# Kernel tuning notes

Measured on AMD Instinct MI355X. Metric: run time of the kernel, lower is better.

Reference implementation:

```python
import jax, jax.numpy as jnp
import numpy as np

B, K, D, NH = 4096, 32, 1024, 16
HD = D // NH
LN_EPS = 1e-5
RMS_EPS = 1e-6


def layernorm(x, g, b):
    mu = jnp.mean(x, axis=-1, keepdims=True)
    var = jnp.mean((x - mu) ** 2, axis=-1, keepdims=True)
    return (x - mu) * jax.lax.rsqrt(var + LN_EPS) * g + b


def rmsnorm(x, g):
    ms = jnp.mean(x ** 2, axis=-1, keepdims=True)
    return x * jax.lax.rsqrt(ms + RMS_EPS) * g


def setup_inputs() -> dict:
    key = jax.random.key(0)
    ks = jax.random.split(key, 12)
    s = 0.02
    inp = {
        "query": jax.random.normal(ks[0], (B, D), jnp.float32),
        "point_features": jax.random.normal(ks[1], (B, K, D), jnp.float32),
        "lnq_g": jnp.ones((D,), jnp.float32),
        "lnq_b": jnp.zeros((D,), jnp.float32),
        "lnkv_g": jnp.ones((D,), jnp.float32),
        "lnkv_b": jnp.zeros((D,), jnp.float32),
        "Wq": jax.random.normal(ks[2], (D, D), jnp.float32) * s,
        "bq": jnp.zeros((D,), jnp.float32),
        "Wk": jax.random.normal(ks[3], (D, D), jnp.float32) * s,
        "bk": jnp.zeros((D,), jnp.float32),
        "Wv": jax.random.normal(ks[4], (D, D), jnp.float32) * s,
        "bv": jnp.zeros((D,), jnp.float32),
        "rmsq_g": jnp.ones((D,), jnp.float32),
        "rmsk_g": jnp.ones((D,), jnp.float32),
        "Wo": jax.random.normal(ks[5], (D, D), jnp.float32) * s,
        "bo": jnp.zeros((D,), jnp.float32),
        "mlpn_g": jnp.ones((D,), jnp.float32),
        "mlpn_b": jnp.zeros((D,), jnp.float32),
        "W1": jax.random.normal(ks[6], (D, 4 * D), jnp.float32) * s,
        "b1": jnp.zeros((4 * D,), jnp.float32),
        "W2": jax.random.normal(ks[7], (4 * D, D), jnp.float32) * s,
        "b2": jnp.zeros((D,), jnp.float32),
    }
    return inp


def reference(query, point_features, lnq_g, lnq_b, lnkv_g, lnkv_b,
              Wq, bq, Wk, bk, Wv, bv, rmsq_g, rmsk_g, Wo, bo,
              mlpn_g, mlpn_b, W1, b1, W2, b2):
    q_in = layernorm(query, lnq_g, lnq_b)            # [B, D]
    kv_in = layernorm(point_features, lnkv_g, lnkv_b)  # [B, K, D]

    q = rmsnorm(q_in @ Wq + bq, rmsq_g)              # [B, D]
    k = rmsnorm(kv_in @ Wk + bk, rmsk_g)             # [B, K, D]
    v = kv_in @ Wv + bv                               # [B, K, D]

    # Faithful to original: raw row-major reshape [B,K,D] -> [B,NH,K,HD]
    qh = q.reshape(B, NH, HD)                         # [B, NH, HD] (q_len = 1)
    kh = k.reshape(B, NH, K, HD)
    vh = v.reshape(B, NH, K, HD)

    scores = jnp.einsum('bhd,bhkd->bhk', qh, kh) / np.sqrt(HD).astype(np.float32)
    attn = jax.nn.softmax(scores, axis=-1)            # [B, NH, K]
    out = jnp.einsum('bhk,bhkd->bhd', attn, vh)       # [B, NH, HD]

    # Faithful: transpose(1,2) then reshape -> [B, HD, NH] -> [B, D]
    out = jnp.transpose(out, (0, 2, 1)).reshape(B, D)
    out = (out @ Wo + bo) + query                     # residual

    h = layernorm(out, mlpn_g, mlpn_b)
    mlp_out = (jax.nn.gelu(h @ W1 + b1, approximate=False) @ W2) + b2
    return out + mlp_out
```

## Files before the change

kernel.cpp:

```cpp
#include <hip/hip_runtime.h>
#include <stdint.h>

#define DEVI __device__ __forceinline__

typedef unsigned short u16;
typedef short s8v __attribute__((ext_vector_type(8)));
typedef float f4v __attribute__((ext_vector_type(4)));
typedef u16 u16x4 __attribute__((ext_vector_type(4)));

DEVI u16 f2bf(float f) {
  unsigned u = __float_as_uint(f);
  u += 0x7fffu + ((u >> 16) & 1u);
  return (u16)(u >> 16);
}
DEVI float bf2f(u16 h) { return __uint_as_float(((unsigned)h) << 16); }

DEVI void gload16(const void* g, void* l) {
  __builtin_amdgcn_global_load_lds(
      (const __attribute__((address_space(1))) void*)(uintptr_t)g,
      (__attribute__((address_space(3))) void*)(uintptr_t)l, 16, 0, 0);
}

__global__ __launch_bounds__(256) void transpose_w(const float* __restrict__ W,
                                                   u16* __restrict__ Wt, int R, int C) {
  __shared__ float tile[32][33];
  const int tx = threadIdx.x & 31, ty = threadIdx.x >> 5;
  const int r0 = blockIdx.y * 32, c0 = blockIdx.x * 32;
#pragma unroll
  for (int i = 0; i < 4; ++i)
    tile[ty + 8 * i][tx] = W[(size_t)(r0 + ty + 8 * i) * C + c0 + tx];
  __syncthreads();
#pragma unroll
  for (int i = 0; i < 4; ++i)
    Wt[(size_t)(c0 + ty + 8 * i) * R + r0 + tx] = f2bf(tile[tx][ty + 8 * i]);
}

__global__ __launch_bounds__(256) void ln_rows(const float* __restrict__ x,
                                               const float* __restrict__ g,
                                               const float* __restrict__ bsh,
                                               u16* __restrict__ y,
                                               float* __restrict__ zbuf) {
  const size_t row = blockIdx.x;
  const int t = threadIdx.x;
  if (zbuf && t == 0) zbuf[row] = 0.f;
  float4 v = ((const float4*)(x + row * 1024))[t];
  float s = v.x + v.y + v.z + v.w;
  float q = v.x * v.x + v.y * v.y + v.z * v.z + v.w * v.w;
#pragma unroll
  for (int m = 1; m < 64; m <<= 1) { s += __shfl_xor(s, m); q += __shfl_xor(q, m); }
  __shared__ float sh[8];
  if ((t & 63) == 0) { sh[t >> 6] = s; sh[4 + (t >> 6)] = q; }
  __syncthreads();
  s = sh[0] + sh[1] + sh[2] + sh[3];
  q = sh[4] + sh[5] + sh[6] + sh[7];
  const float mu = s * (1.f / 1024.f);
  const float var = q * (1.f / 1024.f) - mu * mu;
  const float rs = rsqrtf(var + 1e-5f);
  const int c = t * 4;
  const float in[4] = {v.x, v.y, v.z, v.w};
  u16x4 o;
#pragma unroll
  for (int i = 0; i < 4; ++i) o[i] = f2bf((in[i] - mu) * rs * g[c + i] + bsh[c + i]);
  *(u16x4*)(y + row * 1024 + c) = o;
}

template <int EPI>
__global__ __launch_bounds__(512, 2) void gemm256(
    const u16* __restrict__ A, const u16* __restrict__ Bt,
    const float* __restrict__ biasK, const float* __restrict__ biasV,
    const float* __restrict__ gcol, u16* __restrict__ CK, u16* __restrict__ CV,
    float* __restrict__ rowssq, int M, int N, int K, int RB, int CB) {
  __shared__ u16 lds[4][16384];
  const int t = threadIdx.x;
  const int lane = t & 63;
  const int wave = t >> 6;
  const int wm = wave >> 2, wn = wave & 3;
  const int fr = lane & 15, kq = lane >> 4;

  const int bid = blockIdx.x;
  const int cpx = gridDim.x >> 3;
  const int swz = (bid & 7) * cpx + (bid >> 3);
  const int rb = swz / CB, cb = swz % CB;
  const size_t row0 = (size_t)rb * 256, col0 = (size_t)cb * 256;

  f4v acc[8][4];
#pragma unroll
  for (int i = 0; i < 8; ++i)
#pragma unroll
    for (int n = 0; n < 4; ++n) acc[i][n] = (f4v){0.f, 0.f, 0.f, 0.f};

  const u16* Ag0 = A + (row0 + (t >> 2)) * (size_t)K + (t & 3) * 8;
  const u16* Ag1 = Ag0 + (size_t)128 * K;
  const u16* Bg0 = Bt + (col0 + (t >> 2)) * (size_t)K + (t & 3) * 8;
  const u16* Bg1 = Bg0 + (size_t)128 * K;

  const int NT = K >> 5;

#pragma unroll
  for (int tt = 0; tt < 3; ++tt) {
    u16* sA = &lds[tt][0];
    u16* sB = &lds[tt][8192];
    gload16(Ag0 + tt * 32, sA + t * 8);
    gload16(Ag1 + tt * 32, sA + 4096 + t * 8);
    gload16(Bg0 + tt * 32, sB + t * 8);
    gload16(Bg1 + tt * 32, sB + 4096 + t * 8);
  }

#pragma unroll 4
  for (int T = 0; T < NT; ++T) {
    asm volatile("s_waitcnt vmcnt(8)" ::: "memory");
    __builtin_amdgcn_s_barrier();
    __builtin_amdgcn_sched_barrier(0);
    const u16* sA = &lds[T & 3][0];
    const u16* sB = &lds[T & 3][8192];
    const int Ts = (T + 3 < NT) ? T + 3 : NT - 1;
    s8v a[4], b[4];
#pragma unroll
    for (int m = 0; m < 4; ++m)
      a[m] = *(const s8v*)&sA[(wm * 128 + m * 16 + fr) * 32 + kq * 8];
#pragma unroll
    for (int n = 0; n < 4; ++n)
      b[n] = *(const s8v*)&sB[(wn * 64 + n * 16 + fr) * 32 + kq * 8];
    {
      u16* dA = &lds[(T + 3) & 3][0];
      gload16(Ag0 + Ts * 32, dA + t * 8);
      gload16(Ag1 + Ts * 32, dA + 4096 + t * 8);
    }
    __builtin_amdgcn_s_setprio(1);
#pragma unroll
    for (int m = 0; m < 4; ++m)
#pragma unroll
      for (int n = 0; n < 4; ++n)
        acc[m][n] = __builtin_amdgcn_mfma_f32_16x16x32_bf16(a[m], b[n], acc[m][n], 0, 0, 0);
    __builtin_amdgcn_s_setprio(0);
    __builtin_amdgcn_s_barrier();
#pragma unroll
    for (int m = 0; m < 4; ++m)
      a[m] = *(const s8v*)&sA[(wm * 128 + 64 + m * 16 + fr) * 32 + kq * 8];
    {
      u16* dB = &lds[(T + 3) & 3][8192];
      gload16(Bg0 + Ts * 32, dB + t * 8);
      gload16(Bg1 + Ts * 32, dB + 4096 + t * 8);
    }
    __builtin_amdgcn_s_setprio(1);
#pragma unroll
    for (int m = 0; m < 4; ++m)
#pragma unroll
      for (int n = 0; n < 4; ++n)
        acc[4 + m][n] = __builtin_amdgcn_mfma_f32_16x16x32_bf16(a[m], b[n], acc[4 + m][n], 0, 0, 0);
    __builtin_amdgcn_s_setprio(0);
  }

  const int kq4 = kq * 4;
  if (EPI == 0) {
    const bool isK = (col0 < 1024);
    if (isK) {
#pragma unroll
      for (int ai = 0; ai < 8; ++ai) {
        int cols[4];
        float bb[4], gg[4];
#pragma unroll
        for (int n = 0; n < 4; ++n) {
          cols[n] = (int)col0 + wn * 64 + n * 16 + fr;
          bb[n] = biasK[cols[n]];
          gg[n] = gcol[cols[n]];
        }
#pragma unroll
        for (int r = 0; r < 4; ++r) {
          const size_t grow = row0 + wm * 128 + ai * 16 + kq4 + r;
          float v[4];
#pragma unroll
          for (int n = 0; n < 4; ++n) v[n] = acc[ai][n][r] + bb[n];
          float s = v[0] * v[0] + v[1] * v[1] + v[2] * v[2] + v[3] * v[3];
          s += __shfl_xor(s, 1);
          s += __shfl_xor(s, 2);
          s += __shfl_xor(s, 4);
          s += __shfl_xor(s, 8);
          if (fr == 0) atomicAdd(&rowssq[grow], s);
#pragma unroll
          for (int n = 0; n < 4; ++n)
            CK[grow * 1024 + cols[n]] = f2bf(v[n] * gg[n]);
        }
      }
    } else {
#pragma unroll
      for (int ai = 0; ai < 8; ++ai) {
        int cols[4];
        float bb[4];
#pragma unroll
        for (int n = 0; n < 4; ++n) {
          cols[n] = (int)col0 - 1024 + wn * 64 + n * 16 + fr;
          bb[n] = biasV[cols[n]];
        }
#pragma unroll
        for (int r = 0; r < 4; ++r) {
          const size_t grow = row0 + wm * 128 + ai * 16 + kq4 + r;
#pragma unroll
          for (int n = 0; n < 4; ++n)
            CV[grow * 1024 + cols[n]] = f2bf(acc[ai][n][r] + bb[n]);
        }
      }
    }
  } else {
#pragma unroll
    for (int ai = 0; ai < 8; ++ai) {
      int cols[4];
      float bb[4];
#pragma unroll
      for (int n = 0; n < 4; ++n) {
        cols[n] = (int)col0 + wn * 64 + n * 16 + fr;
        bb[n] = biasK[cols[n]];
      }
#pragma unroll
      for (int r = 0; r < 4; ++r) {
        const size_t grow = row0 + wm * 128 + ai * 16 + kq4 + r;
#pragma unroll
        for (int n = 0; n < 4; ++n) {
          const float x = acc[ai][n][r] + bb[n];
          CK[grow * (size_t)N + cols[n]] = f2bf(0.5f * x * (1.f + erff(x * 0.70710678118654752f)));
        }
      }
    }
  }
}

template <int EPI>
__global__ __launch_bounds__(256) void gemm_bt(
    const u16* __restrict__ A, const u16* __restrict__ Bt,
    const float* __restrict__ bias, const float* __restrict__ gcol,
    void* __restrict__ Cv, const float* __restrict__ extra,
    float* __restrict__ rowssq, int M, int N, int K) {
  __shared__ u16 As[128 * 32];
  __shared__ u16 Bs[128 * 32];
  const int t = threadIdx.x;
  const int lane = t & 63;
  const int wave = t >> 6;
  const int wr = wave >> 1, wc = wave & 1;
  const size_t row0 = (size_t)blockIdx.y * 128;
  const size_t col0 = (size_t)blockIdx.x * 128;
  int Ksub = K, koff = 0;
  if (EPI == 6) { Ksub = K / gridDim.z; koff = blockIdx.z * Ksub; }

  f4v acc[4][4];
#pragma unroll
  for (int m = 0; m < 4; ++m)
#pragma unroll
    for (int n = 0; n < 4; ++n) acc[m][n] = (f4v){0.f, 0.f, 0.f, 0.f};

  const int sr = t >> 2;
  const int sc = (t & 3) * 8;
  const u16* Ag = A + (row0 + sr) * (size_t)K + koff + sc;
  const u16* Bg = Bt + (col0 + sr) * (size_t)K + koff + sc;
  u16* Al = &As[sr * 32 + sc];
  u16* Bl = &Bs[sr * 32 + sc];
  const int fr = lane & 15;
  const int kg = (lane >> 4) * 8;

  for (int k0 = 0; k0 < Ksub; k0 += 32) {
    gload16(Ag + k0, Al);
    gload16(Ag + k0 + (size_t)64 * K, Al + 64 * 32);
    gload16(Bg + k0, Bl);
    gload16(Bg + k0 + (size_t)64 * K, Bl + 64 * 32);
    __syncthreads();
    s8v a[4], b[4];
#pragma unroll
    for (int m = 0; m < 4; ++m)
      a[m] = *(const s8v*)&As[(wr * 64 + m * 16 + fr) * 32 + kg];
#pragma unroll
    for (int n = 0; n < 4; ++n)
      b[n] = *(const s8v*)&Bs[(wc * 64 + n * 16 + fr) * 32 + kg];
#pragma unroll
    for (int m = 0; m < 4; ++m)
#pragma unroll
      for (int n = 0; n < 4; ++n)
        acc[m][n] = __builtin_amdgcn_mfma_f32_16x16x32_bf16(a[m], b[n], acc[m][n], 0, 0, 0);
    __syncthreads();
  }

  float* Cp = (float*)Cv;
  if (EPI == 6) Cp += (size_t)blockIdx.z * M * (size_t)N;
  const int rg = (lane >> 4) * 4;
#pragma unroll
  for (int m = 0; m < 4; ++m) {
    int cols[4];
    float bvals[4];
#pragma unroll
    for (int n = 0; n < 4; ++n) {
      cols[n] = (int)col0 + wc * 64 + n * 16 + fr;
      bvals[n] = (EPI == 6) ? 0.f : bias[cols[n]];
    }
#pragma unroll
    for (int r = 0; r < 4; ++r) {
      const size_t grow = row0 + wr * 64 + m * 16 + rg + r;
      float v[4];
#pragma unroll
      for (int n = 0; n < 4; ++n) v[n] = acc[m][n][r] + bvals[n];
      if (EPI == 5) {
        float s = v[0] * v[0] + v[1] * v[1] + v[2] * v[2] + v[3] * v[3];
        s += __shfl_xor(s, 1);
        s += __shfl_xor(s, 2);
        s += __shfl_xor(s, 4);
        s += __shfl_xor(s, 8);
        if (fr == 0) atomicAdd(&rowssq[grow], s);
      }
#pragma unroll
      for (int n = 0; n < 4; ++n) {
        const size_t idx = grow * (size_t)N + cols[n];
        if (EPI == 3) {
          Cp[idx] = v[n] + extra[idx];
        } else if (EPI == 5) {
          ((u16*)Cv)[idx] = f2bf(v[n]);
        } else if (EPI == 6) {
          Cp[idx] = v[n];
        }
      }
    }
  }
}

__global__ __launch_bounds__(256) void attn_k(const u16* __restrict__ qf,
                                              const u16* __restrict__ kmat,
                                              const float* __restrict__ kssq,
                                              const u16* __restrict__ vmat,
                                              const float* __restrict__ gq,
                                              const float* __restrict__ qssq,
                                              u16* __restrict__ ao) {
  const int lb = blockIdx.x;
  const int t = threadIdx.x;
  const int wave = t >> 6, lane = t & 63;
  const int j = lane & 31, half = lane >> 5;
  const float rq = rsqrtf(qssq[lb] * (1.f / 1024.f) + 1e-6f) * 0.125f;
  __shared__ float po[64][17];
#pragma unroll
  for (int hi = 0; hi < 4; ++hi) {
    const int h = wave * 4 + hi;
    const int krow = lb * 32 + 2 * h + (j >> 4);
    const u16* kp = kmat + (size_t)krow * 1024 + (j & 15) * 64 + half * 32;
    const u16* qp = qf + (size_t)lb * 1024 + h * 64 + half * 32;
    const float* gqp = gq + h * 64 + half * 32;
    float s = 0.f;
#pragma unroll
    for (int cc = 0; cc < 4; ++cc) {
      s8v qv = *(const s8v*)(qp + cc * 8);
      s8v kv = *(const s8v*)(kp + cc * 8);
#pragma unroll
      for (int e = 0; e < 8; ++e)
        s += bf2f((u16)qv[e]) * gqp[cc * 8 + e] * bf2f((u16)kv[e]);
    }
    s += __shfl_xor(s, 32);
    s *= rsqrtf(kssq[krow] * (1.f / 1024.f) + 1e-6f) * rq;
    float mx = s;
#pragma unroll
    for (int m = 16; m >= 1; m >>= 1) mx = fmaxf(mx, __shfl_xor(mx, m));
    const float pe = __expf(s - mx);
    float sum = pe;
#pragma unroll
    for (int m = 16; m >= 1; m >>= 1) sum += __shfl_xor(sum, m);
    const float pr = pe / sum;
    float o = 0.f;
#pragma unroll
    for (int jj = 0; jj < 32; ++jj) {
      const int vrow = lb * 32 + 2 * h + (jj >> 4);
      const float vv = bf2f(vmat[(size_t)vrow * 1024 + (jj & 15) * 64 + lane]);
      o += __shfl(pr, jj) * vv;
    }
    po[lane][h] = o;
  }
  __syncthreads();
  const int c = t * 4;
  u16x4 o4;
#pragma unroll
  for (int i = 0; i < 4; ++i) o4[i] = f2bf(po[(c + i) >> 4][(c + i) & 15]);
  *(u16x4*)(ao + (size_t)lb * 1024 + c) = o4;
}

__global__ __launch_bounds__(256) void combine_k(const float* __restrict__ p0,
                                                 const float* __restrict__ p1,
                                                 const float* __restrict__ b2,
                                                 const float* __restrict__ resid,
                                                 float* __restrict__ out) {
  const int i = blockIdx.x * 256 + threadIdx.x;
  float4 a = ((const float4*)p0)[i];
  float4 b = ((const float4*)p1)[i];
  float4 r = ((const float4*)resid)[i];
  float4 bb = ((const float4*)b2)[i & 255];
  float4 o;
  o.x = a.x + b.x + r.x + bb.x;
  o.y = a.y + b.y + r.y + bb.y;
  o.z = a.z + b.z + r.z + bb.z;
  o.w = a.w + b.w + r.w + bb.w;
  ((float4*)out)[i] = o;
}

extern "C" void kernel_launch(void* const* d_in, const int* in_sizes, int n_in,
                              void* d_out, int out_size, void* d_ws, size_t ws_size,
                              hipStream_t stream) {
  const float* query  = (const float*)d_in[0];
  const float* pf     = (const float*)d_in[1];
  const float* lnq_g  = (const float*)d_in[2];
  const float* lnq_b  = (const float*)d_in[3];
  const float* lnkv_g = (const float*)d_in[4];
  const float* lnkv_b = (const float*)d_in[5];
  const float* Wq     = (const float*)d_in[6];
  const float* bq     = (const float*)d_in[7];
  const float* Wk     = (const float*)d_in[8];
  const float* bk     = (const float*)d_in[9];
  const float* Wv     = (const float*)d_in[10];
  const float* bv     = (const float*)d_in[11];
  const float* rmsq_g = (const float*)d_in[12];
  const float* rmsk_g = (const float*)d_in[13];
  const float* Wo     = (const float*)d_in[14];
  const float* bo     = (const float*)d_in[15];
  const float* mlpn_g = (const float*)d_in[16];
  const float* mlpn_b = (const float*)d_in[17];
  const float* W1     = (const float*)d_in[18];
  const float* b1     = (const float*)d_in[19];
  const float* W2     = (const float*)d_in[20];
  const float* b2     = (const float*)d_in[21];
  float* out = (float*)d_out;

  char* p = (char*)d_ws;
  auto alloc = [&](size_t n) {
    char* r = p;
    p += (n + 255) & ~(size_t)255;
    return r;
  };

  u16* Wqt = (u16*)alloc((size_t)1024 * 1024 * 2);
  u16* KVt = (u16*)alloc((size_t)2048 * 1024 * 2);
  u16* Wot = (u16*)alloc((size_t)1024 * 1024 * 2);
  u16* W1t = (u16*)alloc((size_t)1024 * 4096 * 2);
  u16* W2t = (u16*)alloc((size_t)4096 * 1024 * 2);
  u16* qln = (u16*)alloc((size_t)4096 * 1024 * 2);
  u16* qpre = (u16*)alloc((size_t)4096 * 1024 * 2);
  float* qssq = (float*)alloc((size_t)4096 * 4);
  u16* attn_o = (u16*)alloc((size_t)4096 * 1024 * 2);
  float* outbuf = (float*)alloc((size_t)4096 * 1024 * 4);
  u16* hbuf = (u16*)alloc((size_t)4096 * 1024 * 2);
  u16* mid = (u16*)alloc((size_t)4096 * 4096 * 2);
  float* w2p = (float*)alloc((size_t)2 * 4096 * 1024 * 4);
  const size_t ROWS = 131072;
  u16* kvln = (u16*)alloc(ROWS * 2048);
  u16* kmat = (u16*)alloc(ROWS * 2048);
  u16* vmat = (u16*)alloc(ROWS * 2048);
  float* kssq = (float*)alloc(ROWS * 4);

  transpose_w<<<dim3(32, 32), 256, 0, stream>>>(Wq, Wqt, 1024, 1024);
  transpose_w<<<dim3(32, 32), 256, 0, stream>>>(Wk, KVt, 1024, 1024);
  transpose_w<<<dim3(32, 32), 256, 0, stream>>>(Wv, KVt + (size_t)1024 * 1024, 1024, 1024);
  transpose_w<<<dim3(32, 32), 256, 0, stream>>>(Wo, Wot, 1024, 1024);
  transpose_w<<<dim3(128, 32), 256, 0, stream>>>(W1, W1t, 1024, 4096);
  transpose_w<<<dim3(32, 128), 256, 0, stream>>>(W2, W2t, 4096, 1024);

  ln_rows<<<4096, 256, 0, stream>>>(query, lnq_g, lnq_b, qln, qssq);
  gemm_bt<5><<<dim3(8, 32), 256, 0, stream>>>(qln, Wqt, bq, nullptr, qpre, nullptr,
                                              qssq, 4096, 1024, 1024);

  ln_rows<<<(unsigned)ROWS, 256, 0, stream>>>(pf, lnkv_g, lnkv_b, kvln, kssq);
  gemm256<0><<<512 * 8, 512, 0, stream>>>(kvln, KVt, bk, bv, rmsk_g, kmat, vmat,
                                          kssq, (int)ROWS, 2048, 1024, 512, 8);
  attn_k<<<4096, 256, 0, stream>>>(qpre, kmat, kssq, vmat, rmsq_g, qssq, attn_o);

  gemm_bt<3><<<dim3(8, 32), 256, 0, stream>>>(attn_o, Wot, bo, nullptr, outbuf, query,
                                              nullptr, 4096, 1024, 1024);
  ln_rows<<<4096, 256, 0, stream>>>(outbuf, mlpn_g, mlpn_b, hbuf, nullptr);
  gemm256<1><<<16 * 16, 512, 0, stream>>>(hbuf, W1t, b1, nullptr, nullptr, mid, nullptr,
                                          nullptr, 4096, 4096, 1024, 16, 16);
  gemm_bt<6><<<dim3(8, 32, 2), 256, 0, stream>>>(mid, W2t, nullptr, nullptr, w2p,
                                                 nullptr, nullptr, 4096, 1024, 4096);
  combine_k<<<4096, 256, 0, stream>>>(w2p, w2p + (size_t)4096 * 1024, b2, outbuf, out);
}
```

Before: 1.091 ms.

## XOR-swizzle LDS tile layout in GEMMs and merge main-loop MFMA phases

Global-to-LDS loads now pick a swizzled source column chunk, (t&3)^((row>>1)&3), so each row's 16-byte k-chunks land permuted in LDS. Fragment reads use the matching XOR index, which is meant to remove LDS bank conflicts on the ds_read_b128 fragment loads in both GEMM kernels. The large GEMM's loop also drops its mid-iteration barrier: all A and B fragments are loaded up front, both prefetches are issued together, and the two MFMA groups run back to back. This trades more live VGPRs and less interleaving of loads with compute for fewer barriers.

Measured after the change: 1.103 ms. Within noise of the previous version (+1.1%).

```diff
diff --git a/kernel.cpp b/kernel.cpp
--- a/kernel.cpp
+++ b/kernel.cpp
@@ -89,10 +89,14 @@
 #pragma unroll
     for (int n = 0; n < 4; ++n) acc[i][n] = (f4v){0.f, 0.f, 0.f, 0.f};
 
-  const u16* Ag0 = A + (row0 + (t >> 2)) * (size_t)K + (t & 3) * 8;
+  const int srow = t >> 2;
+  const int scol = (((t & 3) ^ ((t >> 3) & 3)) << 3);
+  const u16* Ag0 = A + (row0 + srow) * (size_t)K + scol;
   const u16* Ag1 = Ag0 + (size_t)128 * K;
-  const u16* Bg0 = Bt + (col0 + (t >> 2)) * (size_t)K + (t & 3) * 8;
+  const u16* Bg0 = Bt + (col0 + srow) * (size_t)K + scol;
   const u16* Bg1 = Bg0 + (size_t)128 * K;
+
+  const int kx = ((kq ^ ((fr >> 1) & 3)) << 3);
 
   const int NT = K >> 5;
 
@@ -114,31 +118,21 @@
     const u16* sA = &lds[T & 3][0];
     const u16* sB = &lds[T & 3][8192];
     const int Ts = (T + 3 < NT) ? T + 3 : NT - 1;
-    s8v a[4], b[4];
-#pragma unroll
-    for (int m = 0; m < 4; ++m)
-      a[m] = *(const s8v*)&sA[(wm * 128 + m * 16 + fr) * 32 + kq * 8];
+    s8v a0[4], a1[4], b[4];
+#pragma unroll
+    for (int m = 0; m < 4; ++m)
+      a0[m] = *(const s8v*)&sA[(wm * 128 + m * 16 + fr) * 32 + kx];
 #pragma unroll
     for (int n = 0; n < 4; ++n)
-      b[n] = *(const s8v*)&sB[(wn * 64 + n * 16 + fr) * 32 + kq * 8];
+      b[n] = *(const s8v*)&sB[(wn * 64 + n * 16 + fr) * 32 + kx];
+#pragma unroll
+    for (int m = 0; m < 4; ++m)
+      a1[m] = *(const s8v*)&sA[(wm * 128 + 64 + m * 16 + fr) * 32 + kx];
     {
       u16* dA = &lds[(T + 3) & 3][0];
+      u16* dB = &lds[(T + 3) & 3][8192];
       gload16(Ag0 + Ts * 32, dA + t * 8);
       gload16(Ag1 + Ts * 32, dA + 4096 + t * 8);
-    }
-    __builtin_amdgcn_s_setprio(1);
-#pragma unroll
-    for (int m = 0; m < 4; ++m)
-#pragma unroll
-      for (int n = 0; n < 4; ++n)
-        acc[m][n] = __builtin_amdgcn_mfma_f32_16x16x32_bf16(a[m], b[n], acc[m][n], 0, 0, 0);
-    __builtin_amdgcn_s_setprio(0);
-    __builtin_amdgcn_s_barrier();
-#pragma unroll
-    for (int m = 0; m < 4; ++m)
-      a[m] = *(const s8v*)&sA[(wm * 128 + 64 + m * 16 + fr) * 32 + kq * 8];
-    {
-      u16* dB = &lds[(T + 3) & 3][8192];
       gload16(Bg0 + Ts * 32, dB + t * 8);
       gload16(Bg1 + Ts * 32, dB + 4096 + t * 8);
     }
@@ -147,7 +141,12 @@
     for (int m = 0; m < 4; ++m)
 #pragma unroll
       for (int n = 0; n < 4; ++n)
-        acc[4 + m][n] = __builtin_amdgcn_mfma_f32_16x16x32_bf16(a[m], b[n], acc[4 + m][n], 0, 0, 0);
+        acc[m][n] = __builtin_amdgcn_mfma_f32_16x16x32_bf16(a0[m], b[n], acc[m][n], 0, 0, 0);
+#pragma unroll
+    for (int m = 0; m < 4; ++m)
+#pragma unroll
+      for (int n = 0; n < 4; ++n)
+        acc[4 + m][n] = __builtin_amdgcn_mfma_f32_16x16x32_bf16(a1[m], b[n], acc[4 + m][n], 0, 0, 0);
     __builtin_amdgcn_s_setprio(0);
   }
 
@@ -248,13 +247,13 @@
     for (int n = 0; n < 4; ++n) acc[m][n] = (f4v){0.f, 0.f, 0.f, 0.f};
 
   const int sr = t >> 2;
-  const int sc = (t & 3) * 8;
-  const u16* Ag = A + (row0 + sr) * (size_t)K + koff + sc;
-  const u16* Bg = Bt + (col0 + sr) * (size_t)K + koff + sc;
-  u16* Al = &As[sr * 32 + sc];
-  u16* Bl = &Bs[sr * 32 + sc];
+  const int scw = (((t & 3) ^ ((t >> 3) & 3)) << 3);
+  const u16* Ag = A + (row0 + sr) * (size_t)K + koff + scw;
+  const u16* Bg = Bt + (col0 + sr) * (size_t)K + koff + scw;
+  u16* Al = &As[t * 8];
+  u16* Bl = &Bs[t * 8];
   const int fr = lane & 15;
-  const int kg = (lane >> 4) * 8;
+  const int kx = (((lane >> 4) ^ ((fr >> 1) & 3)) << 3);
 
   for (int k0 = 0; k0 < Ksub; k0 += 32) {
     gload16(Ag + k0, Al);
@@ -265,10 +264,10 @@
     s8v a[4], b[4];
 #pragma unroll
     for (int m = 0; m < 4; ++m)
-      a[m] = *(const s8v*)&As[(wr * 64 + m * 16 + fr) * 32 + kg];
+      a[m] = *(const s8v*)&As[(wr * 64 + m * 16 + fr) * 32 + kx];
 #pragma unroll
     for (int n = 0; n < 4; ++n)
-      b[n] = *(const s8v*)&Bs[(wc * 64 + n * 16 + fr) * 32 + kg];
+      b[n] = *(const s8v*)&Bs[(wc * 64 + n * 16 + fr) * 32 + kx];
 #pragma unroll
     for (int m = 0; m < 4; ++m)
 #pragma unroll
```
